# Kernel tuning notes

Measured on AMD Instinct MI355X. Metric: run time of the kernel, lower is better.

Reference implementation:

```python
import jax, jax.numpy as jnp
import numpy as np

N, IN, D, H = 65536, 512, 256, 4  # nodes, in_channels, out_channels (per head), num_heads


def setup_inputs() -> dict:
    key = jax.random.key(0)
    ks = jax.random.split(key, 8)
    s = 1.0 / np.sqrt(IN)  # torch nn.Linear default init range
    def lin(kw, kb):
        W = jax.random.uniform(kw, (IN, H * D), jnp.float32, -s, s)
        b = jax.random.uniform(kb, (H * D,), jnp.float32, -s, s)
        return W, b
    Wq, bq = lin(ks[0], ks[1])
    Wk, bk = lin(ks[2], ks[3])
    Wv, bv = lin(ks[4], ks[5])
    x = jax.random.normal(ks[6], (N, IN), jnp.float32)
    n_nodes = jnp.array([N], jnp.int32)  # single graph; unused when block_wise=False
    return {"x": x, "Wq": Wq, "bq": bq, "Wk": Wk, "bk": bk, "Wv": Wv, "bv": bv,
            "n_nodes": n_nodes}


def reference(x, Wq, bq, Wk, bk, Wv, bv, n_nodes):
    # Projections -> [N, H, D]
    q = (x @ Wq + bq).reshape(N, H, D)
    k = (x @ Wk + bk).reshape(N, H, D)
    v = (x @ Wv + bv).reshape(N, H, D)
    # L2-normalize q, k per head (kernel='simple')
    qn = q / jnp.linalg.norm(q, axis=-1, keepdims=True)
    kn = k / jnp.linalg.norm(k, axis=-1, keepdims=True)
    # Linear attention: K^T V then Q @ (KV), all heads at once
    kv = jnp.einsum('nhm,nhd->hmd', kn, v)                    # [H, D, D]
    num = jnp.einsum('nhm,hmd->nhd', qn, kv) + v.sum(axis=0)  # [N, H, D]
    ksum = kn.sum(axis=0)                                     # [H, D]
    denom = jnp.einsum('nhm,hm->nh', qn, ksum) + jnp.float32(N)  # [N, H]
    out = num / denom[..., None]
    return out.mean(axis=1)  # mean over heads -> [N, D]
```

## Files before the change

### kernel.cpp

```cpp
#include <hip/hip_runtime.h>

#define NNODES 65536
#define INC    512
#define NH     4
#define HD     256
#define HDTOT  1024

typedef __bf16 bf16_t;
typedef __bf16 bf16x4_t __attribute__((ext_vector_type(4)));
typedef __bf16 bf16x8_t __attribute__((ext_vector_type(8)));
typedef float  f32x4_t  __attribute__((ext_vector_type(4)));

__device__ __forceinline__ bf16_t f2bf(float f) { return (bf16_t)f; }

__device__ __forceinline__ void gl_lds16(const void* g, void* l) {
  __builtin_amdgcn_global_load_lds(
      (const __attribute__((address_space(1))) void*)g,
      (__attribute__((address_space(3))) void*)l, 16, 0, 0);
}

__global__ void k0_wt(const float* __restrict__ Wq, const float* __restrict__ Wk,
                      const float* __restrict__ Wv, bf16_t* __restrict__ Wt) {
  __shared__ float tile[32][33];
  int mat = blockIdx.z;
  const float* W = (mat == 0) ? Wq : (mat == 1) ? Wk : Wv;
  int n0 = blockIdx.x * 32, k0 = blockIdx.y * 32;
  int t = threadIdx.x, tc = t & 31, tr = t >> 5;
#pragma unroll
  for (int i = 0; i < 4; ++i)
    tile[tr + i * 8][tc] = W[(size_t)(k0 + tr + i * 8) * HDTOT + n0 + tc];
  __syncthreads();
#pragma unroll
  for (int i = 0; i < 4; ++i)
    Wt[((size_t)mat * HDTOT + n0 + tr + i * 8) * INC + k0 + tc] =
        f2bf(tile[tc][tr + i * 8]);
}

__global__ void k0b_xb(const float* __restrict__ x, bf16_t* __restrict__ xb) {
  size_t i = ((size_t)blockIdx.x * 256 + threadIdx.x) * 8;
  float4 a = *(const float4*)(x + i);
  float4 b = *(const float4*)(x + i + 4);
  bf16x8_t o;
  o[0] = f2bf(a.x); o[1] = f2bf(a.y); o[2] = f2bf(a.z); o[3] = f2bf(a.w);
  o[4] = f2bf(b.x); o[5] = f2bf(b.y); o[6] = f2bf(b.z); o[7] = f2bf(b.w);
  *(bf16x8_t*)(xb + i) = o;
}

__global__ __launch_bounds__(512, 4) void k1_qkv(
    const bf16_t* __restrict__ xb, const bf16_t* __restrict__ Wt,
    const float* __restrict__ bq, const float* __restrict__ bk,
    const float* __restrict__ bv,
    bf16_t* __restrict__ qn, bf16_t* __restrict__ knT2, bf16_t* __restrict__ vT2,
    float* __restrict__ ksum, float* __restrict__ vsum) {
  __shared__ __align__(16) char smem[52224];
  bf16_t* ept  = (bf16_t*)smem;
  float* sred  = (float*)(smem + 49152);
  float* sredc = (float*)(smem + 51200);

  const int gxy = blockIdx.x;
  const int mat = gxy >> 2, head = gxy & 3;
  const int n0 = blockIdx.y * 128;
  const int t = threadIdx.x;
  const int wid = t >> 6, lane = t & 63;
  const int l15 = lane & 15, l4 = lane >> 4;
  const int wr = wid >> 2, wc = wid & 3;

  const f32x4_t zero4 = {0.f, 0.f, 0.f, 0.f};
  f32x4_t acc[4][4];
#pragma unroll
  for (int i = 0; i < 4; ++i)
#pragma unroll
    for (int j = 0; j < 4; ++j) acc[i][j] = zero4;

  const char* Ab = (const char*)(xb + (size_t)n0 * INC);
  const char* Bb = (const char*)(Wt + ((size_t)mat * HDTOT + head * HD) * INC);

  auto stage = [&](int kt, int c) {
    const int kb = kt * 64;
    {
      int o = t * 16, r = o >> 6, cb = o & 63;
      gl_lds16(Ab + (size_t)r * 1024 + kb + (cb ^ ((r & 3) << 4)), smem + c * 8192 + o);
    }
#pragma unroll
    for (int i = 0; i < 2; ++i) {
      int o = i * 8192 + t * 16, r = o >> 6, cb = o & 63;
      gl_lds16(Bb + (size_t)r * 1024 + kb + (cb ^ ((r & 3) << 4)),
               smem + 16384 + c * 16384 + o);
    }
  };

  stage(0, 0);
  __syncthreads();
  int cur = 0;
  for (int kt = 0; kt < 16; ++kt) {
    if (kt < 15) stage(kt + 1, cur ^ 1);
    const char* lA = smem + cur * 8192;
    const char* lB = smem + 16384 + cur * 16384;
    bf16x8_t af[4], bfr[4];
#pragma unroll
    for (int i = 0; i < 4; ++i) {
      int r = wr * 64 + i * 16 + l15;
      af[i] = *(const bf16x8_t*)(lA + r * 64 + ((l4 * 16) ^ ((r & 3) << 4)));
    }
#pragma unroll
    for (int j = 0; j < 4; ++j) {
      int r = wc * 64 + j * 16 + l15;
      bfr[j] = *(const bf16x8_t*)(lB + r * 64 + ((l4 * 16) ^ ((r & 3) << 4)));
    }
    __builtin_amdgcn_s_setprio(1);
#pragma unroll
    for (int i = 0; i < 4; ++i)
#pragma unroll
      for (int j = 0; j < 4; ++j)
        acc[i][j] = __builtin_amdgcn_mfma_f32_16x16x32_bf16(af[i], bfr[j], acc[i][j], 0, 0, 0);
    __builtin_amdgcn_s_setprio(0);
    __syncthreads();
    cur ^= 1;
  }

  const float* bias = (mat == 0) ? bq : (mat == 1) ? bk : bv;
#pragma unroll
  for (int jf = 0; jf < 4; ++jf) {
    float bb = bias[head * HD + wc * 64 + jf * 16 + l15];
#pragma unroll
    for (int i = 0; i < 4; ++i)
#pragma unroll
      for (int jj = 0; jj < 4; ++jj) acc[i][jf][jj] += bb;
  }

  if (mat <= 1) {
    float ss[4][4];
#pragma unroll
    for (int i = 0; i < 4; ++i)
#pragma unroll
      for (int jj = 0; jj < 4; ++jj) {
        float s = 0.f;
#pragma unroll
        for (int jf = 0; jf < 4; ++jf) s += acc[i][jf][jj] * acc[i][jf][jj];
        ss[i][jj] = s;
      }
#pragma unroll
    for (int off = 1; off < 16; off <<= 1)
#pragma unroll
      for (int i = 0; i < 4; ++i)
#pragma unroll
        for (int jj = 0; jj < 4; ++jj) ss[i][jj] += __shfl_xor(ss[i][jj], off, 64);
    if (l15 == 0) {
#pragma unroll
      for (int i = 0; i < 4; ++i)
#pragma unroll
        for (int jj = 0; jj < 4; ++jj)
          sred[(wr * 64 + i * 16 + l4 * 4 + jj) * 4 + wc] = ss[i][jj];
    }
    __syncthreads();
#pragma unroll
    for (int i = 0; i < 4; ++i)
#pragma unroll
      for (int jj = 0; jj < 4; ++jj) {
        int row = wr * 64 + i * 16 + l4 * 4 + jj;
        float s = sred[row * 4] + sred[row * 4 + 1] + sred[row * 4 + 2] + sred[row * 4 + 3];
        float rn = rsqrtf(s);
#pragma unroll
        for (int jf = 0; jf < 4; ++jf) acc[i][jf][jj] *= rn;
      }
  }

  if (mat >= 1) {
    float cs[4];
#pragma unroll
    for (int jf = 0; jf < 4; ++jf) {
      float s = 0.f;
#pragma unroll
      for (int i = 0; i < 4; ++i)
#pragma unroll
        for (int jj = 0; jj < 4; ++jj) s += acc[i][jf][jj];
      s += __shfl_xor(s, 16, 64);
      s += __shfl_xor(s, 32, 64);
      cs[jf] = s;
    }
    if (t < 256) sredc[t] = 0.f;
    __syncthreads();
    if (l4 == 0) {
#pragma unroll
      for (int jf = 0; jf < 4; ++jf)
        atomicAdd(&sredc[wc * 64 + jf * 16 + l15], cs[jf]);
    }
    __syncthreads();
    float* dstSum = (mat == 1) ? ksum : vsum;
    if (t < 256) atomicAdd(dstSum + head * HD + t, sredc[t]);
  }

  const int ldp = (mat == 0) ? 264 : 258;
  for (int ph = 0; ph < 2; ++ph) {
    __syncthreads();
    if (wr == ph) {
#pragma unroll
      for (int i = 0; i < 4; ++i)
#pragma unroll
        for (int jf = 0; jf < 4; ++jf)
#pragma unroll
          for (int jj = 0; jj < 4; ++jj)
            ept[(i * 16 + l4 * 4 + jj) * ldp + wc * 64 + jf * 16 + l15] =
                f2bf(acc[i][jf][jj]);
    }
    __syncthreads();
    const int hn0 = n0 + ph * 64;
    if (mat == 0) {
#pragma unroll
      for (int i = 0; i < 4; ++i) {
        int idx = t + i * 512;
        int r = idx >> 5, c8 = (idx & 31) * 8;
        *(bf16x8_t*)(qn + (size_t)(hn0 + r) * HDTOT + head * HD + c8) =
            *(const bf16x8_t*)(ept + r * 264 + c8);
      }
    } else {
      int m = t & 255, seg = t >> 8;
      bf16_t* dst = (mat == 1) ? knT2 : vT2;
      unsigned int pack[16];
#pragma unroll
      for (int rr = 0; rr < 32; rr += 2) {
        int r = seg * 32 + rr;
        unsigned int a = *(const unsigned short*)(ept + r * 258 + m);
        unsigned int b = *(const unsigned short*)(ept + (r + 1) * 258 + m);
        pack[rr >> 1] = a | (b << 16);
      }
      size_t base = ((((size_t)(head * 2 + (m >> 7)) * 1024 + (hn0 >> 6)) * 128 +
                      (m & 127)) * 64) + seg * 32;
      uint4* dp = (uint4*)(dst + base);
#pragma unroll
      for (int i = 0; i < 4; ++i)
        dp[i] = make_uint4(pack[i * 4], pack[i * 4 + 1], pack[i * 4 + 2], pack[i * 4 + 3]);
    }
  }
}

__global__ __launch_bounds__(256, 4) void k2_kv(
    const bf16_t* __restrict__ knT2, const bf16_t* __restrict__ vT2,
    float* __restrict__ kvP) {
  __shared__ __align__(16) char smem[65536];

  const int gx = blockIdx.x;
  const int head = blockIdx.y, ch = blockIdx.z;
  const int td = gx >> 1, tm = gx & 1;

  const int t = threadIdx.x, wid = t >> 6, lane = t & 63;
  const int l15 = lane & 15, l4 = lane >> 4;
  const int wr = wid >> 1, wc = wid & 1;

  const f32x4_t zero4 = {0.f, 0.f, 0.f, 0.f};
  f32x4_t acc[4][4];
#pragma unroll
  for (int i = 0; i < 4; ++i)
#pragma unroll
    for (int j = 0; j < 4; ++j) acc[i][j] = zero4;

  const char* Abase = (const char*)vT2  + ((size_t)(head * 2 + td) * 1024 + ch * 32) * 16384;
  const char* Bbase = (const char*)knT2 + ((size_t)(head * 2 + tm) * 1024 + ch * 32) * 16384;

  auto stage = [&](int it, int c) {
#pragma unroll
    for (int i = 0; i < 4; ++i) {
      int o = i * 4096 + t * 16, r = o >> 7, cb = o & 127;
      int so = r * 128 + (cb ^ ((r & 7) << 4));
      gl_lds16(Abase + (size_t)it * 16384 + so, smem + c * 16384 + o);
      gl_lds16(Bbase + (size_t)it * 16384 + so, smem + 32768 + c * 16384 + o);
    }
  };

  stage(0, 0);
  __syncthreads();
  int cur = 0;
  for (int it = 0; it < 32; ++it) {
    if (it < 31) stage(it + 1, cur ^ 1);
    const char* lA = smem + cur * 16384;
    const char* lB = smem + 32768 + cur * 16384;
#pragma unroll
    for (int ks = 0; ks < 2; ++ks) {
      bf16x8_t af[4], bfr[4];
#pragma unroll
      for (int i = 0; i < 4; ++i) {
        int r = wr * 64 + i * 16 + l15;
        af[i] = *(const bf16x8_t*)(lA + r * 128 + ((ks * 64 + l4 * 16) ^ ((r & 7) << 4)));
      }
#pragma unroll
      for (int j = 0; j < 4; ++j) {
        int r = wc * 64 + j * 16 + l15;
        bfr[j] = *(const bf16x8_t*)(lB + r * 128 + ((ks * 64 + l4 * 16) ^ ((r & 7) << 4)));
      }
      __builtin_amdgcn_s_setprio(1);
#pragma unroll
      for (int i = 0; i < 4; ++i)
#pragma unroll
        for (int j = 0; j < 4; ++j)
          acc[i][j] = __builtin_amdgcn_mfma_f32_16x16x32_bf16(af[i], bfr[j], acc[i][j], 0, 0, 0);
      __builtin_amdgcn_s_setprio(0);
    }
    __syncthreads();
    cur ^= 1;
  }

  float* dst = kvP + ((size_t)(ch * 16 + head * 4 + gx)) * 16384;
#pragma unroll
  for (int i = 0; i < 4; ++i)
#pragma unroll
    for (int jj = 0; jj < 4; ++jj)
#pragma unroll
      for (int j = 0; j < 4; ++j)
        dst[(wr * 64 + i * 16 + l4 * 4 + j) * 128 + wc * 64 + jj * 16 + l15] =
            acc[i][jj][j];
}

__global__ void k3_red(const float* __restrict__ kvP, bf16_t* __restrict__ kvTb) {
  int tid = blockIdx.x * 256 + threadIdx.x;
  int base = tid * 4;
  int m = base & 255, d = (base >> 8) & 255, h = base >> 16;
  int gx = ((d >> 7) << 1) | (m >> 7);
  int off = (d & 127) * 128 + (m & 127);
  f32x4_t s = {0.f, 0.f, 0.f, 0.f};
#pragma unroll
  for (int ch = 0; ch < 32; ++ch)
    s += *(const f32x4_t*)(kvP + (((size_t)(ch * 16 + h * 4 + gx)) << 14) + off);
  bf16x4_t b;
  b[0] = f2bf(s[0]); b[1] = f2bf(s[1]); b[2] = f2bf(s[2]); b[3] = f2bf(s[3]);
  *(bf16x4_t*)(kvTb + (size_t)base) = b;
}

__global__ __launch_bounds__(256, 2) void k4_out(
    const bf16_t* __restrict__ qn, const bf16_t* __restrict__ kvTb,
    const float* __restrict__ ksum, const float* __restrict__ vsum,
    float* __restrict__ out) {
  __shared__ __align__(16) char smem[66560];
  float* sdn = (float*)(smem + 65536);

  const int n0 = blockIdx.x * 64;
  const int t = threadIdx.x, wid = t >> 6, lane = t & 63;
  const int l15 = lane & 15, l4 = lane >> 4;

  const f32x4_t zero4 = {0.f, 0.f, 0.f, 0.f};
  f32x4_t oacc[16];
#pragma unroll
  for (int f = 0; f < 16; ++f) oacc[f] = zero4;

  const char* qb  = (const char*)qn + (size_t)n0 * 2048;
  const char* kvb = (const char*)kvTb;

  for (int h = 0; h < NH; ++h) {
#pragma unroll
    for (int i = 0; i < 8; ++i) {
      int o = i * 4096 + t * 16, r = o >> 9, cb = o & 511;
      int scb = (cb & 0x180) | ((cb & 0x7F) ^ ((r & 7) << 4));
      gl_lds16(qb + (size_t)r * 2048 + h * 512 + scb, smem + o);
    }
    f32x4_t hacc[16];
#pragma unroll
    for (int f = 0; f < 16; ++f) hacc[f] = zero4;
    float dnp = 0.f;

    for (int mc = 0; mc < 4; ++mc) {
#pragma unroll
      for (int i = 0; i < 8; ++i) {
        int o = i * 4096 + t * 16, r = o >> 7, cb = o & 127;
        gl_lds16(kvb + (size_t)h * 131072 + (size_t)r * 512 + mc * 128 +
                     (cb ^ ((r & 7) << 4)),
                 smem + 32768 + o);
      }
      __syncthreads();
      if (mc == 0) {
        int r = t & 63, qd = t >> 6;
        float s = 0.f;
#pragma unroll
        for (int j = 0; j < 64; ++j) {
          int cb2 = (qd * 64 + j) * 2;
          int a = r * 512 + ((cb2 & 0x180) | ((cb2 & 0x7F) ^ ((r & 7) << 4)));
          s += (float)(*(const bf16_t*)(smem + a)) * ksum[h * HD + qd * 64 + j];
        }
        dnp = s;
      }
#pragma unroll
      for (int ks = 0; ks < 2; ++ks) {
        int ra = wid * 16 + l15;
        bf16x8_t af = *(const bf16x8_t*)(
            smem + ra * 512 + ((mc * 128 + ks * 64 + l4 * 16) ^ ((ra & 7) << 4)));
        __builtin_amdgcn_s_setprio(1);
#pragma unroll
        for (int f = 0; f < 16; ++f) {
          int rb = f * 16 + l15;
          bf16x8_t bfr = *(const bf16x8_t*)(
              smem + 32768 + rb * 128 + ((ks * 64 + l4 * 16) ^ ((rb & 7) << 4)));
          hacc[f] = __builtin_amdgcn_mfma_f32_16x16x32_bf16(af, bfr, hacc[f], 0, 0, 0);
        }
        __builtin_amdgcn_s_setprio(0);
      }
      __syncthreads();
    }
    sdn[t] = dnp;
    __syncthreads();
    if (t < 64)
      sdn[t] = 1.0f / (sdn[t] + sdn[t + 64] + sdn[t + 128] + sdn[t + 192] + 65536.0f);
    __syncthreads();
    float rdn[4];
#pragma unroll
    for (int j = 0; j < 4; ++j) rdn[j] = sdn[wid * 16 + l4 * 4 + j];
#pragma unroll
    for (int f = 0; f < 16; ++f) {
      float vs = vsum[h * HD + f * 16 + l15];
#pragma unroll
      for (int j = 0; j < 4; ++j) oacc[f][j] += (hacc[f][j] + vs) * rdn[j];
    }
    __syncthreads();
  }
#pragma unroll
  for (int f = 0; f < 16; ++f)
#pragma unroll
    for (int j = 0; j < 4; ++j)
      out[(size_t)(n0 + wid * 16 + l4 * 4 + j) * HD + f * 16 + l15] =
          oacc[f][j] * 0.25f;
}

extern "C" void kernel_launch(void* const* d_in, const int* in_sizes, int n_in,
                              void* d_out, int out_size, void* d_ws, size_t ws_size,
                              hipStream_t stream) {
  const float* x  = (const float*)d_in[0];
  const float* Wq = (const float*)d_in[1];
  const float* bq = (const float*)d_in[2];
  const float* Wk = (const float*)d_in[3];
  const float* bk = (const float*)d_in[4];
  const float* Wv = (const float*)d_in[5];
  const float* bv = (const float*)d_in[6];
  float* out = (float*)d_out;
  char* ws = (char*)d_ws;

  bf16_t* qn   = (bf16_t*)(ws);
  bf16_t* knT2 = (bf16_t*)(ws + 134217728L);
  bf16_t* vT2  = (bf16_t*)(ws + 268435456L);
  bf16_t* Wt   = (bf16_t*)(ws + 402653184L);
  bf16_t* kvTb = (bf16_t*)(ws + 406847488L);
  float*  ksum = (float*) (ws + 407371776L);
  float*  vsum = (float*) (ws + 407375872L);
  bf16_t* xb   = (bf16_t*)(ws + 407379968L);
  float*  kvP  = (float*) (ws + 407379968L);

  hipMemsetAsync(ksum, 0, 8192, stream);

  k0_wt  <<<dim3(32, 16, 3), 256, 0, stream>>>(Wq, Wk, Wv, Wt);
  k0b_xb <<<dim3(16384),     256, 0, stream>>>(x, xb);
  k1_qkv <<<dim3(12, 512),   512, 0, stream>>>(xb, Wt, bq, bk, bv, qn, knT2, vT2, ksum, vsum);
  k2_kv  <<<dim3(4, 4, 32),  256, 0, stream>>>(knT2, vT2, kvP);
  k3_red <<<dim3(256),       256, 0, stream>>>(kvP, kvTb);
  k4_out <<<dim3(1024),      256, 0, stream>>>(qn, kvTb, ksum, vsum, out);
}
```

Baseline: 665.0 us.

## Deepen global-to-LDS prefetch pipelines and remap QKV blocks for XCD locality

Reworks the k1 and k2 GEMM loops to issue loads two stages ahead, using explicit vmcnt waits and raw barriers instead of __syncthreads. This keeps more loads in flight across the barrier. k4 gets a double-buffered KV tile, prefetches the next head's Q and KV tiles, and goes to one block per CU with more LDS. The k1 grid becomes 1-D and is remapped so each XCD handles a contiguous range of rows across all 12 mat/head tiles, which should improve L2 reuse of x. The risks are lower occupancy in k4 and fragile hand-written waitcnt counts.

```diff
diff --git a/kernel.cpp b/kernel.cpp
--- a/kernel.cpp
+++ b/kernel.cpp
@@ -57,9 +57,11 @@
   float* sred  = (float*)(smem + 49152);
   float* sredc = (float*)(smem + 51200);
 
-  const int gxy = blockIdx.x;
+  const int bid = blockIdx.x;
+  const int xcd = bid & 7, pos = bid >> 3;
+  const int gxy = pos % 12;
   const int mat = gxy >> 2, head = gxy & 3;
-  const int n0 = blockIdx.y * 128;
+  const int n0 = (xcd * 64 + pos / 12) * 128;
   const int t = threadIdx.x;
   const int wid = t >> 6, lane = t & 63;
   const int l15 = lane & 15, l4 = lane >> 4;
@@ -90,10 +92,13 @@
   };
 
   stage(0, 0);
-  __syncthreads();
-  int cur = 0;
+  stage(1, 1);
   for (int kt = 0; kt < 16; ++kt) {
-    if (kt < 15) stage(kt + 1, cur ^ 1);
+    const int cur = kt & 1;
+    if (kt == 15) asm volatile("s_waitcnt vmcnt(0)" ::: "memory");
+    else          asm volatile("s_waitcnt vmcnt(3)" ::: "memory");
+    __builtin_amdgcn_s_barrier();
+    __builtin_amdgcn_sched_barrier(0);
     const char* lA = smem + cur * 8192;
     const char* lB = smem + 16384 + cur * 16384;
     bf16x8_t af[4], bfr[4];
@@ -114,8 +119,9 @@
       for (int j = 0; j < 4; ++j)
         acc[i][j] = __builtin_amdgcn_mfma_f32_16x16x32_bf16(af[i], bfr[j], acc[i][j], 0, 0, 0);
     __builtin_amdgcn_s_setprio(0);
-    __syncthreads();
-    cur ^= 1;
+    __builtin_amdgcn_s_barrier();
+    __builtin_amdgcn_sched_barrier(0);
+    if (kt < 14) stage(kt + 2, cur);
   }
 
   const float* bias = (mat == 0) ? bq : (mat == 1) ? bk : bv;
@@ -268,10 +274,13 @@
   };
 
   stage(0, 0);
-  __syncthreads();
-  int cur = 0;
+  stage(1, 1);
   for (int it = 0; it < 32; ++it) {
-    if (it < 31) stage(it + 1, cur ^ 1);
+    const int cur = it & 1;
+    if (it == 31) asm volatile("s_waitcnt vmcnt(0)" ::: "memory");
+    else          asm volatile("s_waitcnt vmcnt(8)" ::: "memory");
+    __builtin_amdgcn_s_barrier();
+    __builtin_amdgcn_sched_barrier(0);
     const char* lA = smem + cur * 16384;
     const char* lB = smem + 32768 + cur * 16384;
 #pragma unroll
@@ -295,8 +304,9 @@
           acc[i][j] = __builtin_amdgcn_mfma_f32_16x16x32_bf16(af[i], bfr[j], acc[i][j], 0, 0, 0);
       __builtin_amdgcn_s_setprio(0);
     }
-    __syncthreads();
-    cur ^= 1;
+    __builtin_amdgcn_s_barrier();
+    __builtin_amdgcn_sched_barrier(0);
+    if (it < 30) stage(it + 2, cur);
   }
 
   float* dst = kvP + ((size_t)(ch * 16 + head * 4 + gx)) * 16384;
@@ -325,12 +335,12 @@
   *(bf16x4_t*)(kvTb + (size_t)base) = b;
 }
 
-__global__ __launch_bounds__(256, 2) void k4_out(
+__global__ __launch_bounds__(256, 1) void k4_out(
     const bf16_t* __restrict__ qn, const bf16_t* __restrict__ kvTb,
     const float* __restrict__ ksum, const float* __restrict__ vsum,
     float* __restrict__ out) {
-  __shared__ __align__(16) char smem[66560];
-  float* sdn = (float*)(smem + 65536);
+  __shared__ __align__(16) char smem[99584];
+  float* sdn = (float*)(smem + 98304);
 
   const int n0 = blockIdx.x * 64;
   const int t = threadIdx.x, wid = t >> 6, lane = t & 63;
@@ -344,27 +354,38 @@
   const char* qb  = (const char*)qn + (size_t)n0 * 2048;
   const char* kvb = (const char*)kvTb;
 
-  for (int h = 0; h < NH; ++h) {
+  auto stage_la = [&](int h) {
 #pragma unroll
     for (int i = 0; i < 8; ++i) {
       int o = i * 4096 + t * 16, r = o >> 9, cb = o & 511;
       int scb = (cb & 0x180) | ((cb & 0x7F) ^ ((r & 7) << 4));
       gl_lds16(qb + (size_t)r * 2048 + h * 512 + scb, smem + o);
     }
+  };
+  auto stage_lb = [&](int h, int mc, int buf) {
+#pragma unroll
+    for (int i = 0; i < 8; ++i) {
+      int o = i * 4096 + t * 16, r = o >> 7, cb = o & 127;
+      gl_lds16(kvb + (size_t)h * 131072 + (size_t)r * 512 + mc * 128 +
+                   (cb ^ ((r & 7) << 4)),
+               smem + 32768 + buf * 32768 + o);
+    }
+  };
+
+  stage_la(0);
+  stage_lb(0, 0, 0);
+  for (int h = 0; h < NH; ++h) {
     f32x4_t hacc[16];
 #pragma unroll
     for (int f = 0; f < 16; ++f) hacc[f] = zero4;
     float dnp = 0.f;
 
     for (int mc = 0; mc < 4; ++mc) {
-#pragma unroll
-      for (int i = 0; i < 8; ++i) {
-        int o = i * 4096 + t * 16, r = o >> 7, cb = o & 127;
-        gl_lds16(kvb + (size_t)h * 131072 + (size_t)r * 512 + mc * 128 +
-                     (cb ^ ((r & 7) << 4)),
-                 smem + 32768 + o);
-      }
-      __syncthreads();
+      const int cur = mc & 1;
+      asm volatile("s_waitcnt vmcnt(0)" ::: "memory");
+      __builtin_amdgcn_s_barrier();
+      __builtin_amdgcn_sched_barrier(0);
+      if (mc < 3) stage_lb(h, mc + 1, cur ^ 1);
       if (mc == 0) {
         int r = t & 63, qd = t >> 6;
         float s = 0.f;
@@ -376,6 +397,7 @@
         }
         dnp = s;
       }
+      const char* lb = smem + 32768 + cur * 32768;
 #pragma unroll
       for (int ks = 0; ks < 2; ++ks) {
         int ra = wid * 16 + l15;
@@ -386,12 +408,13 @@
         for (int f = 0; f < 16; ++f) {
           int rb = f * 16 + l15;
           bf16x8_t bfr = *(const bf16x8_t*)(
-              smem + 32768 + rb * 128 + ((ks * 64 + l4 * 16) ^ ((rb & 7) << 4)));
+              lb + rb * 128 + ((ks * 64 + l4 * 16) ^ ((rb & 7) << 4)));
           hacc[f] = __builtin_amdgcn_mfma_f32_16x16x32_bf16(af, bfr, hacc[f], 0, 0, 0);
         }
         __builtin_amdgcn_s_setprio(0);
       }
-      __syncthreads();
+      __builtin_amdgcn_s_barrier();
+      __builtin_amdgcn_sched_barrier(0);
     }
     sdn[t] = dnp;
     __syncthreads();
@@ -408,6 +431,11 @@
       for (int j = 0; j < 4; ++j) oacc[f][j] += (hacc[f][j] + vs) * rdn[j];
     }
     __syncthreads();
+    __builtin_amdgcn_sched_barrier(0);
+    if (h < 3) {
+      stage_la(h + 1);
+      stage_lb(h + 1, 0, 0);
+    }
   }
 #pragma unroll
   for (int f = 0; f < 16; ++f)
@@ -444,7 +472,7 @@
 
   k0_wt  <<<dim3(32, 16, 3), 256, 0, stream>>>(Wq, Wk, Wv, Wt);
   k0b_xb <<<dim3(16384),     256, 0, stream>>>(x, xb);
-  k1_qkv <<<dim3(12, 512),   512, 0, stream>>>(xb, Wt, bq, bk, bv, qn, knT2, vT2, ksum, vsum);
+  k1_qkv <<<dim3(6144),      512, 0, stream>>>(xb, Wt, bq, bk, bv, qn, knT2, vT2, ksum, vsum);
   k2_kv  <<<dim3(4, 4, 32),  256, 0, stream>>>(knT2, vT2, kvP);
   k3_red <<<dim3(256),       256, 0, stream>>>(kvP, kvTb);
   k4_out <<<dim3(1024),      256, 0, stream>>>(qn, kvTb, ksum, vsum, out);
```

Result: slower. 713.7 us (+7.3%).
